# Optimization experiments

Measured on AMD Instinct MI355X. Metric: run time of the kernel, lower is better.

Reference implementation:

```python
import jax, jax.numpy as jnp
import numpy as np

B, D_MODEL, L = 4, 512, 1024
N_HEADS = 8

def setup_inputs() -> dict:
    key = jax.random.key(0)
    ks = jax.random.split(key, 7)
    s = 1.0 / np.sqrt(D_MODEL)
    return {
        "queries": jax.random.normal(ks[0], (B, D_MODEL, 3, L), dtype=jnp.float32),
        "keys":    jax.random.normal(ks[1], (B, D_MODEL, 3, L), dtype=jnp.float32),
        "values":  jax.random.normal(ks[2], (B, D_MODEL, 3, L), dtype=jnp.float32),
        "Wq": jax.random.normal(ks[3], (D_MODEL, D_MODEL), dtype=jnp.float32) * s,
        "Wk": jax.random.normal(ks[4], (D_MODEL, D_MODEL), dtype=jnp.float32) * s,
        "Wv": jax.random.normal(ks[5], (D_MODEL, D_MODEL), dtype=jnp.float32) * s,
        "Wo": jax.random.normal(ks[6], (D_MODEL, D_MODEL), dtype=jnp.float32) * s,
        "n_heads": N_HEADS,
    }

def reference(queries, keys, values, Wq, Wk, Wv, Wo, n_heads):
    # inputs: [B, D, 3, L]; VNLinear = bias-free linear over channel dim D
    Bv, D, _, Lv = queries.shape
    H = n_heads
    dh = D // H
    # project and reshape to [B, L, H, dh, 3]
    def proj(x, W):
        y = jnp.einsum('ed,bdvl->blev', W, x)          # [B, L, D, 3]
        return y.reshape(Bv, Lv, H, dh, 3)
    q = proj(queries, Wq)
    k = proj(keys, Wk)
    v = proj(values, Wv)
    # score over extra vector axis v: [B, H, 3, L, S]
    score = jnp.einsum('blhdv,bshdv->bhvls', q, k)
    scale = 1.0 / jnp.sqrt(jnp.asarray(3.0, score.dtype))  # original grabs last dim (=3)
    attn = jax.nn.softmax(scale * score, axis=-1)
    # weighted values: [B, L, 3, H, dh] -> [B, L, 3, D]
    V = jnp.einsum('bhvls,bshdv->blvhd', attn, v).reshape(Bv, Lv, 3, D)
    # output projection on channel dim: result [B, D, 3, L]
    out = jnp.einsum('ed,blvd->bevl', Wo, V)
    return out, attn
```

## Files before the change

kernel.cpp:

```cpp
#include <hip/hip_runtime.h>
#include <hip/hip_bf16.h>

typedef __hip_bfloat16 bf16;
using bf16x8 = __attribute__((ext_vector_type(8))) short;
using f32x4  = __attribute__((ext_vector_type(4))) float;

#define Bn 4
#define Dm 512
#define Hh 8
#define V3 3
#define Lq 1024
#define NM (Bn*Hh*V3)

#define WPITCH 144

__device__ __forceinline__ unsigned short f2bf(float x) {
    bf16 h = __float2bfloat16(x);
    return *reinterpret_cast<unsigned short*>(&h);
}
__device__ __forceinline__ float bfbits2f(unsigned short u) {
    return __uint_as_float((unsigned)u << 16);
}

constexpr float SCALE = 0.57735026919f;

__global__ __launch_bounds__(256, 4) void proj_all_kernel(
    const float* __restrict__ xq, const float* __restrict__ xk,
    const float* __restrict__ xv,
    const float* __restrict__ Wq, const float* __restrict__ Wk,
    const float* __restrict__ Wv,
    unsigned short* __restrict__ Qh, unsigned short* __restrict__ Ql,
    unsigned short* __restrict__ Kh, unsigned short* __restrict__ Kl,
    unsigned short* __restrict__ Vt)
{
    __shared__ unsigned char Wlds[2 * 64 * WPITCH];
    unsigned char* LWh = Wlds;
    unsigned char* LWl = Wlds + 64 * WPITCH;

    const int fid = (blockIdx.z * gridDim.y + blockIdx.y) * gridDim.x + blockIdx.x;
    const int nid = (fid & 7) * 576 + (fid >> 3);
    const int x_  = nid & 15;
    const int y_  = (nid >> 4) & 7;
    const int zz  = nid >> 7;
    const int pid = zz / 12;
    const int pl  = zz % 12;
    const int b   = pl / V3;
    const int v   = pl % V3;

    const float* xsrc = (pid == 0) ? xq : (pid == 1) ? xk : xv;
    const float* W    = (pid == 0) ? Wq : (pid == 1) ? Wk : Wv;

    const int l0 = x_ * 64;
    const int e0 = y_ * 64;
    const int m  = (b * Hh + y_) * V3 + v;

    const int tid  = threadIdx.x;
    const int w    = tid >> 6;
    const int ln   = tid & 63;
    const int ln15 = ln & 15;
    const int lq   = ln >> 4;
    const int wl   = w * 16 + ln15;

    const float* xbase = xsrc + (size_t)b * Dm * V3 * Lq + (size_t)v * Lq + l0 + wl;

    f32x4 acc[4];
    #pragma unroll
    for (int i = 0; i < 4; ++i) acc[i] = (f32x4)0.f;

    for (int ph = 0; ph < 8; ++ph) {
        const int d0 = ph * 64;

        float xraw[16];
        #pragma unroll
        for (int kq = 0; kq < 2; ++kq)
            #pragma unroll
            for (int j = 0; j < 8; ++j)
                xraw[kq * 8 + j] =
                    xbase[(size_t)(d0 + kq * 32 + lq * 8 + j) * (V3 * Lq)];

        __syncthreads();
        #pragma unroll
        for (int q2 = 0; q2 < 4; ++q2) {
            int idx  = tid + q2 * 256;
            int row  = idx >> 4;
            int dloc = (idx & 15) * 4;
            float4 wv4 = *reinterpret_cast<const float4*>(
                W + (size_t)(e0 + row) * Dm + d0 + dloc);
            float wz[4] = {wv4.x, wv4.y, wv4.z, wv4.w};
            union { unsigned short u[4]; uint2 v2; } hp, lp;
            #pragma unroll
            for (int e = 0; e < 4; ++e) {
                hp.u[e] = f2bf(wz[e]);
                lp.u[e] = f2bf(wz[e] - bfbits2f(hp.u[e]));
            }
            *reinterpret_cast<uint2*>(LWh + row * WPITCH + dloc * 2) = hp.v2;
            *reinterpret_cast<uint2*>(LWl + row * WPITCH + dloc * 2) = lp.v2;
        }
        __syncthreads();

        bf16x8 xh[2], xl[2];
        #pragma unroll
        for (int kq = 0; kq < 2; ++kq)
            #pragma unroll
            for (int j = 0; j < 8; ++j) {
                float xv_ = xraw[kq * 8 + j];
                unsigned short hs = f2bf(xv_);
                unsigned short ls = f2bf(xv_ - bfbits2f(hs));
                xh[kq][j] = (short)hs;
                xl[kq][j] = (short)ls;
            }

        #pragma unroll
        for (int lt = 0; lt < 4; ++lt) {
            int erow = lt * 16 + ln15;
            #pragma unroll
            for (int kq = 0; kq < 2; ++kq) {
                bf16x8 wh = *reinterpret_cast<const bf16x8*>(
                    LWh + erow * WPITCH + kq * 64 + lq * 16);
                bf16x8 wl_ = *reinterpret_cast<const bf16x8*>(
                    LWl + erow * WPITCH + kq * 64 + lq * 16);
                acc[lt] = __builtin_amdgcn_mfma_f32_16x16x32_bf16(wh,  xh[kq], acc[lt], 0, 0, 0);
                acc[lt] = __builtin_amdgcn_mfma_f32_16x16x32_bf16(wl_, xh[kq], acc[lt], 0, 0, 0);
                acc[lt] = __builtin_amdgcn_mfma_f32_16x16x32_bf16(wh,  xl[kq], acc[lt], 0, 0, 0);
            }
        }
    }

    if (pid < 2) {
        unsigned short* Oh_ = (pid == 0) ? Qh : Kh;
        unsigned short* Ol_ = (pid == 0) ? Ql : Kl;
        size_t rowbase = ((size_t)m * Lq + l0 + wl) * 64;
        #pragma unroll
        for (int lt = 0; lt < 4; ++lt) {
            union { unsigned short u[4]; uint2 v2; } hp, lp;
            #pragma unroll
            for (int r = 0; r < 4; ++r) {
                float y = acc[lt][r];
                hp.u[r] = f2bf(y);
                lp.u[r] = f2bf(y - bfbits2f(hp.u[r]));
            }
            *reinterpret_cast<uint2*>(Oh_ + rowbase + lt * 16 + lq * 4) = hp.v2;
            *reinterpret_cast<uint2*>(Ol_ + rowbase + lt * 16 + lq * 4) = lp.v2;
        }
    } else {
        #pragma unroll
        for (int lt = 0; lt < 4; ++lt)
            #pragma unroll
            for (int r = 0; r < 4; ++r) {
                int dd = lt * 16 + lq * 4 + r;
                Vt[(((size_t)(m * 64 + dd)) << 10) + l0 + wl] = f2bf(acc[lt][r]);
            }
    }
}

__device__ __forceinline__ void stage_tile64(
    unsigned char* dst, const unsigned short* __restrict__ src,
    size_t row_stride, int tid)
{
    #pragma unroll
    for (int q = 0; q < 2; ++q) {
        int u = tid + q * 256;
        int row = u >> 3, off = u & 7;
        uint4 d = *reinterpret_cast<const uint4*>(src + (size_t)row * row_stride + off * 8);
        *reinterpret_cast<uint4*>(dst + ((row * 128 + off * 16) ^ ((row & 7) << 4))) = d;
    }
}

__global__ __launch_bounds__(256) void fused_attn_kernel(
    const unsigned short* __restrict__ Qh, const unsigned short* __restrict__ Ql,
    const unsigned short* __restrict__ Kh, const unsigned short* __restrict__ Kl,
    const unsigned short* __restrict__ Vt, float* __restrict__ attn_out,
    unsigned short* __restrict__ Ot)
{
    __shared__ float4 ldsf4[2128];
    unsigned char* L   = (unsigned char*)ldsf4;
    unsigned char* Lkh = L;
    unsigned char* Lkl = L + 8192;
    unsigned char* Lvt = L + 16384;
    unsigned char* Lp  = L + 24576;
    float* rowsumW = (float*)(L + 32768);
    float* invrow  = (float*)(L + 33792);

    const int fid = blockIdx.y * gridDim.x + blockIdx.x;
    const int nid = (fid & 7) * 192 + (fid >> 3);
    const int m  = nid >> 4;
    const int l0 = (nid & 15) * 64;

    const int tid = threadIdx.x;
    const int w    = tid >> 6;
    const int ln   = tid & 63;
    const int ln15 = ln & 15;
    const int lq   = ln >> 4;
    const int sc   = w * 16;

    stage_tile64(Lkh, Qh + ((size_t)m * Lq + l0) * 64, 64, tid);
    stage_tile64(Lkl, Ql + ((size_t)m * Lq + l0) * 64, 64, tid);
    __syncthreads();
    bf16x8 qfh[4][2], qfl[4][2];
    #pragma unroll
    for (int lt = 0; lt < 4; ++lt) {
        int row = lt * 16 + ln15;
        #pragma unroll
        for (int kq = 0; kq < 2; ++kq) {
            int byte = (row * 128 + kq * 64 + lq * 16) ^ ((row & 7) << 4);
            qfh[lt][kq] = *reinterpret_cast<const bf16x8*>(Lkh + byte);
            qfl[lt][kq] = *reinterpret_cast<const bf16x8*>(Lkl + byte);
        }
    }
    __syncthreads();

    const size_t mbase = (size_t)m * Lq * Lq;
    const unsigned short* Khm = Kh + (size_t)m * Lq * 64;
    const unsigned short* Klm = Kl + (size_t)m * Lq * 64;
    const unsigned short* Vtm = Vt + (((size_t)m * 64) << 10);

    float lsum[4][4] = {};
    for (int s0 = 0; s0 < Lq; s0 += 64) {
        stage_tile64(Lkh, Khm + (size_t)s0 * 64, 64, tid);
        stage_tile64(Lkl, Klm + (size_t)s0 * 64, 64, tid);
        __syncthreads();
        bf16x8 bh[2], bl[2];
        #pragma unroll
        for (int kq = 0; kq < 2; ++kq) {
            int row = sc + ln15;
            int byte = (row * 128 + kq * 64 + lq * 16) ^ ((row & 7) << 4);
            bh[kq] = *reinterpret_cast<const bf16x8*>(Lkh + byte);
            bl[kq] = *reinterpret_cast<const bf16x8*>(Lkl + byte);
        }
        #pragma unroll
        for (int lt = 0; lt < 4; ++lt) {
            f32x4 c = (f32x4)0.f;
            #pragma unroll
            for (int kq = 0; kq < 2; ++kq) {
                c = __builtin_amdgcn_mfma_f32_16x16x32_bf16(qfh[lt][kq], bh[kq], c, 0, 0, 0);
                c = __builtin_amdgcn_mfma_f32_16x16x32_bf16(qfl[lt][kq], bh[kq], c, 0, 0, 0);
                c = __builtin_amdgcn_mfma_f32_16x16x32_bf16(qfh[lt][kq], bl[kq], c, 0, 0, 0);
            }
            #pragma unroll
            for (int r = 0; r < 4; ++r)
                lsum[lt][r] += __expf(c[r] * SCALE);
        }
        __syncthreads();
    }
    #pragma unroll
    for (int lt = 0; lt < 4; ++lt)
        #pragma unroll
        for (int r = 0; r < 4; ++r) {
            float vv = lsum[lt][r];
            vv += __shfl_xor(vv, 1);
            vv += __shfl_xor(vv, 2);
            vv += __shfl_xor(vv, 4);
            vv += __shfl_xor(vv, 8);
            if (ln15 == 0) rowsumW[w * 64 + lt * 16 + lq * 4 + r] = vv;
        }
    __syncthreads();
    if (tid < 64)
        invrow[tid] = 1.0f / (rowsumW[tid] + rowsumW[64 + tid] +
                              rowsumW[128 + tid] + rowsumW[192 + tid]);
    __syncthreads();

    f32x4 o[4];
    o[0] = (f32x4)0.f; o[1] = (f32x4)0.f; o[2] = (f32x4)0.f; o[3] = (f32x4)0.f;

    const int arow = tid >> 2;
    const int acb  = (tid & 3) * 32;
    const int aswz = (arow & 7) << 4;

    for (int s0 = 0; s0 < Lq; s0 += 64) {
        stage_tile64(Lkh, Khm + (size_t)s0 * 64, 64, tid);
        stage_tile64(Lkl, Klm + (size_t)s0 * 64, 64, tid);
        stage_tile64(Lvt, Vtm + s0, 1024, tid);
        __syncthreads();
        bf16x8 bh[2], bl[2];
        #pragma unroll
        for (int kq = 0; kq < 2; ++kq) {
            int row = sc + ln15;
            int byte = (row * 128 + kq * 64 + lq * 16) ^ ((row & 7) << 4);
            bh[kq] = *reinterpret_cast<const bf16x8*>(Lkh + byte);
            bl[kq] = *reinterpret_cast<const bf16x8*>(Lkl + byte);
        }
        #pragma unroll
        for (int lt = 0; lt < 4; ++lt) {
            f32x4 c = (f32x4)0.f;
            #pragma unroll
            for (int kq = 0; kq < 2; ++kq) {
                c = __builtin_amdgcn_mfma_f32_16x16x32_bf16(qfh[lt][kq], bh[kq], c, 0, 0, 0);
                c = __builtin_amdgcn_mfma_f32_16x16x32_bf16(qfl[lt][kq], bh[kq], c, 0, 0, 0);
                c = __builtin_amdgcn_mfma_f32_16x16x32_bf16(qfh[lt][kq], bl[kq], c, 0, 0, 0);
            }
            #pragma unroll
            for (int r = 0; r < 4; ++r) {
                int l = lt * 16 + lq * 4 + r;
                float p = __expf(c[r] * SCALE) * invrow[l];
                int byte = (l * 128 + (sc + ln15) * 2) ^ ((l & 7) << 4);
                *reinterpret_cast<unsigned short*>(Lp + byte) = f2bf(p);
            }
        }
        __syncthreads();
        {
            int prow = w * 16 + ln15;
            #pragma unroll
            for (int kq = 0; kq < 2; ++kq) {
                bf16x8 pa = *reinterpret_cast<const bf16x8*>(
                    Lp + ((prow * 128 + kq * 64 + lq * 16) ^ ((prow & 7) << 4)));
                #pragma unroll
                for (int nt = 0; nt < 4; ++nt) {
                    int vrow = nt * 16 + ln15;
                    bf16x8 vb = *reinterpret_cast<const bf16x8*>(
                        Lvt + ((vrow * 128 + kq * 64 + lq * 16) ^ ((vrow & 7) << 4)));
                    o[nt] = __builtin_amdgcn_mfma_f32_16x16x32_bf16(pa, vb, o[nt], 0, 0, 0);
                }
            }
        }
        {
            bf16x8 p0 = *reinterpret_cast<const bf16x8*>(
                Lp + ((arow * 128 + acb) ^ aswz));
            bf16x8 p1 = *reinterpret_cast<const bf16x8*>(
                Lp + ((arow * 128 + acb + 16) ^ aswz));
            float* dst = attn_out + mbase + (size_t)(l0 + arow) * Lq + s0 + (tid & 3) * 16;
            float4 f;
            f.x = bfbits2f((unsigned short)p0[0]);
            f.y = bfbits2f((unsigned short)p0[1]);
            f.z = bfbits2f((unsigned short)p0[2]);
            f.w = bfbits2f((unsigned short)p0[3]);
            *reinterpret_cast<float4*>(dst) = f;
            f.x = bfbits2f((unsigned short)p0[4]);
            f.y = bfbits2f((unsigned short)p0[5]);
            f.z = bfbits2f((unsigned short)p0[6]);
            f.w = bfbits2f((unsigned short)p0[7]);
            *reinterpret_cast<float4*>(dst + 4) = f;
            f.x = bfbits2f((unsigned short)p1[0]);
            f.y = bfbits2f((unsigned short)p1[1]);
            f.z = bfbits2f((unsigned short)p1[2]);
            f.w = bfbits2f((unsigned short)p1[3]);
            *reinterpret_cast<float4*>(dst + 8) = f;
            f.x = bfbits2f((unsigned short)p1[4]);
            f.y = bfbits2f((unsigned short)p1[5]);
            f.z = bfbits2f((unsigned short)p1[6]);
            f.w = bfbits2f((unsigned short)p1[7]);
            *reinterpret_cast<float4*>(dst + 12) = f;
        }
        __syncthreads();
    }

    #pragma unroll
    for (int nt = 0; nt < 4; ++nt) {
        int dd = nt * 16 + ln15;
        #pragma unroll
        for (int r = 0; r < 4; ++r) {
            int l = w * 16 + lq * 4 + r;
            Ot[((size_t)m * Lq + l0 + l) * 64 + dd] = f2bf(o[nt][r]);
        }
    }
}

__global__ __launch_bounds__(256, 4) void oproj_kernel(
    const float* __restrict__ Wo, const unsigned short* __restrict__ Ot,
    float* __restrict__ out)
{
    __shared__ unsigned char Wlds[2 * 64 * WPITCH];
    unsigned char* LWh = Wlds;
    unsigned char* LWl = Wlds + 64 * WPITCH;

    const int fid = (blockIdx.z * gridDim.y + blockIdx.y) * gridDim.x + blockIdx.x;
    const int nid = (fid & 7) * 192 + (fid >> 3);
    const int x_  = nid & 15;
    const int y_  = (nid >> 4) & 7;
    const int pl  = nid >> 7;
    const int b   = pl / V3;
    const int v   = pl % V3;

    const int l0 = x_ * 64;
    const int e0 = y_ * 64;

    const int tid  = threadIdx.x;
    const int w    = tid >> 6;
    const int ln   = tid & 63;
    const int ln15 = ln & 15;
    const int lq   = ln >> 4;
    const int wl   = w * 16 + ln15;

    f32x4 acc[4];
    #pragma unroll
    for (int i = 0; i < 4; ++i) acc[i] = (f32x4)0.f;

    for (int h = 0; h < Hh; ++h) {
        const int m = (b * Hh + h) * V3 + v;

        size_t obase = ((size_t)m * Lq + l0 + wl) * 64;
        bf16x8 ob0 = *reinterpret_cast<const bf16x8*>(Ot + obase + lq * 8);
        bf16x8 ob1 = *reinterpret_cast<const bf16x8*>(Ot + obase + 32 + lq * 8);

        __syncthreads();
        #pragma unroll
        for (int q2 = 0; q2 < 4; ++q2) {
            int idx  = tid + q2 * 256;
            int row  = idx >> 4;
            int dloc = (idx & 15) * 4;
            float4 wv4 = *reinterpret_cast<const float4*>(
                Wo + (size_t)(e0 + row) * Dm + h * 64 + dloc);
            float wz[4] = {wv4.x, wv4.y, wv4.z, wv4.w};
            union { unsigned short u[4]; uint2 v2; } hp, lp;
            #pragma unroll
            for (int e = 0; e < 4; ++e) {
                hp.u[e] = f2bf(wz[e]);
                lp.u[e] = f2bf(wz[e] - bfbits2f(hp.u[e]));
            }
            *reinterpret_cast<uint2*>(LWh + row * WPITCH + dloc * 2) = hp.v2;
            *reinterpret_cast<uint2*>(LWl + row * WPITCH + dloc * 2) = lp.v2;
        }
        __syncthreads();

        #pragma unroll
        for (int lt = 0; lt < 4; ++lt) {
            int erow = lt * 16 + ln15;
            #pragma unroll
            for (int kq = 0; kq < 2; ++kq) {
                bf16x8 wh = *reinterpret_cast<const bf16x8*>(
                    LWh + erow * WPITCH + kq * 64 + lq * 16);
                bf16x8 wl_ = *reinterpret_cast<const bf16x8*>(
                    LWl + erow * WPITCH + kq * 64 + lq * 16);
                bf16x8 ob = kq ? ob1 : ob0;
                acc[lt] = __builtin_amdgcn_mfma_f32_16x16x32_bf16(wh,  ob, acc[lt], 0, 0, 0);
                acc[lt] = __builtin_amdgcn_mfma_f32_16x16x32_bf16(wl_, ob, acc[lt], 0, 0, 0);
            }
        }
    }

    #pragma unroll
    for (int lt = 0; lt < 4; ++lt)
        #pragma unroll
        for (int r = 0; r < 4; ++r) {
            int e = e0 + lt * 16 + lq * 4 + r;
            out[((size_t)(b * Dm + e) * V3 + v) * Lq + l0 + wl] = acc[lt][r];
        }
}

extern "C" void kernel_launch(void* const* d_in, const int* in_sizes, int n_in,
                              void* d_out, int out_size, void* d_ws, size_t ws_size,
                              hipStream_t stream)
{
    const float* q  = (const float*)d_in[0];
    const float* k  = (const float*)d_in[1];
    const float* vv = (const float*)d_in[2];
    const float* Wq = (const float*)d_in[3];
    const float* Wk = (const float*)d_in[4];
    const float* Wv = (const float*)d_in[5];
    const float* Wo = (const float*)d_in[6];

    float* out      = (float*)d_out;
    float* attn_out = out + (size_t)Bn * Dm * V3 * Lq;

    char* w = (char*)d_ws;
    unsigned short* Qh = (unsigned short*)(w);
    unsigned short* Ql = (unsigned short*)(w + 12582912);
    unsigned short* Kh = (unsigned short*)(w + 25165824);
    unsigned short* Kl = (unsigned short*)(w + 37748736);
    unsigned short* Vt = (unsigned short*)(w + 50331648);
    unsigned short* Ot = (unsigned short*)(w + 62914560);

    dim3 b256(256);

    proj_all_kernel<<<dim3(16, 8, 36), b256, 0, stream>>>(
        q, k, vv, Wq, Wk, Wv, Qh, Ql, Kh, Kl, Vt);

    fused_attn_kernel<<<dim3(16, NM), b256, 0, stream>>>(
        Qh, Ql, Kh, Kl, Vt, attn_out, Ot);

    oproj_kernel<<<dim3(16, 8, 12), b256, 0, stream>>>(Wo, Ot, out);
}
```

Measured before the change: 721.7 us.

## Pre-split weights once and share K/V tiles across two query blocks

A new kernel splits all four weight matrices into bf16 hi/lo planes once per call. The projection kernels then copy pre-split bf16 tiles into LDS instead of converting fp32 weights in every block. The attention kernel now uses 512-thread blocks that cover 128 query rows as two 64-row halves, so each staged K/V tile serves twice as many queries and global K/V traffic is halved. This adds a kernel launch and uses more LDS per block, which may lower occupancy.

```diff
diff --git a/kernel.cpp b/kernel.cpp
--- a/kernel.cpp
+++ b/kernel.cpp
@@ -24,11 +24,31 @@
 
 constexpr float SCALE = 0.57735026919f;
 
+__global__ __launch_bounds__(256) void split_w_kernel(
+    const float* __restrict__ Wq, const float* __restrict__ Wk,
+    const float* __restrict__ Wv, const float* __restrict__ Wo,
+    unsigned short* __restrict__ Wsp)
+{
+    const int mi = blockIdx.x >> 8;
+    const float* src = (mi == 0) ? Wq : (mi == 1) ? Wk : (mi == 2) ? Wv : Wo;
+    const int idx = ((blockIdx.x & 255) << 8) + threadIdx.x;
+    float4 v4 = reinterpret_cast<const float4*>(src)[idx];
+    float z[4] = {v4.x, v4.y, v4.z, v4.w};
+    union { unsigned short u[4]; uint2 q; } hp, lp;
+    #pragma unroll
+    for (int e = 0; e < 4; ++e) {
+        hp.u[e] = f2bf(z[e]);
+        lp.u[e] = f2bf(z[e] - bfbits2f(hp.u[e]));
+    }
+    unsigned short* hi = Wsp + (size_t)mi * 524288;
+    *reinterpret_cast<uint2*>(hi + (size_t)idx * 4)          = hp.q;
+    *reinterpret_cast<uint2*>(hi + 262144 + (size_t)idx * 4) = lp.q;
+}
+
 __global__ __launch_bounds__(256, 4) void proj_all_kernel(
     const float* __restrict__ xq, const float* __restrict__ xk,
     const float* __restrict__ xv,
-    const float* __restrict__ Wq, const float* __restrict__ Wk,
-    const float* __restrict__ Wv,
+    const unsigned short* __restrict__ Wsp,
     unsigned short* __restrict__ Qh, unsigned short* __restrict__ Ql,
     unsigned short* __restrict__ Kh, unsigned short* __restrict__ Kl,
     unsigned short* __restrict__ Vt)
@@ -48,7 +68,8 @@
     const int v   = pl % V3;
 
     const float* xsrc = (pid == 0) ? xq : (pid == 1) ? xk : xv;
-    const float* W    = (pid == 0) ? Wq : (pid == 1) ? Wk : Wv;
+    const unsigned short* WhX = Wsp + (size_t)pid * 524288;
+    const unsigned short* WlX = WhX + 262144;
 
     const int l0 = x_ * 64;
     const int e0 = y_ * 64;
@@ -81,20 +102,14 @@
         __syncthreads();
         #pragma unroll
         for (int q2 = 0; q2 < 4; ++q2) {
-            int idx  = tid + q2 * 256;
-            int row  = idx >> 4;
-            int dloc = (idx & 15) * 4;
-            float4 wv4 = *reinterpret_cast<const float4*>(
-                W + (size_t)(e0 + row) * Dm + d0 + dloc);
-            float wz[4] = {wv4.x, wv4.y, wv4.z, wv4.w};
-            union { unsigned short u[4]; uint2 v2; } hp, lp;
-            #pragma unroll
-            for (int e = 0; e < 4; ++e) {
-                hp.u[e] = f2bf(wz[e]);
-                lp.u[e] = f2bf(wz[e] - bfbits2f(hp.u[e]));
-            }
-            *reinterpret_cast<uint2*>(LWh + row * WPITCH + dloc * 2) = hp.v2;
-            *reinterpret_cast<uint2*>(LWl + row * WPITCH + dloc * 2) = lp.v2;
+            int idx = tid + q2 * 256;
+            const unsigned short* srcw = (idx < 512) ? WhX : WlX;
+            unsigned char* dstw = (idx < 512) ? LWh : LWl;
+            int i = idx & 511;
+            int row = i >> 3, off = i & 7;
+            uint4 d = *reinterpret_cast<const uint4*>(
+                srcw + (size_t)(e0 + row) * Dm + d0 + off * 8);
+            *reinterpret_cast<uint4*>(dstw + row * WPITCH + off * 16) = d;
         }
         __syncthreads();
 
@@ -153,49 +168,54 @@
     }
 }
 
-__device__ __forceinline__ void stage_tile64(
+__device__ __forceinline__ void stage512(
     unsigned char* dst, const unsigned short* __restrict__ src,
     size_t row_stride, int tid)
 {
-    #pragma unroll
-    for (int q = 0; q < 2; ++q) {
-        int u = tid + q * 256;
-        int row = u >> 3, off = u & 7;
-        uint4 d = *reinterpret_cast<const uint4*>(src + (size_t)row * row_stride + off * 8);
-        *reinterpret_cast<uint4*>(dst + ((row * 128 + off * 16) ^ ((row & 7) << 4))) = d;
-    }
-}
-
-__global__ __launch_bounds__(256) void fused_attn_kernel(
+    int row = tid >> 3, off = tid & 7;
+    uint4 d = *reinterpret_cast<const uint4*>(src + (size_t)row * row_stride + off * 8);
+    *reinterpret_cast<uint4*>(dst + ((row * 128 + off * 16) ^ ((row & 7) << 4))) = d;
+}
+
+__global__ __launch_bounds__(512, 4) void fused_attn_kernel(
     const unsigned short* __restrict__ Qh, const unsigned short* __restrict__ Ql,
     const unsigned short* __restrict__ Kh, const unsigned short* __restrict__ Kl,
     const unsigned short* __restrict__ Vt, float* __restrict__ attn_out,
     unsigned short* __restrict__ Ot)
 {
-    __shared__ float4 ldsf4[2128];
+    __shared__ float4 ldsf4[2720];
     unsigned char* L   = (unsigned char*)ldsf4;
     unsigned char* Lkh = L;
     unsigned char* Lkl = L + 8192;
     unsigned char* Lvt = L + 16384;
     unsigned char* Lp  = L + 24576;
-    float* rowsumW = (float*)(L + 32768);
-    float* invrow  = (float*)(L + 33792);
+    float* rowsumW = (float*)(L + 40960);
+    float* invrow  = (float*)(L + 43008);
 
     const int fid = blockIdx.y * gridDim.x + blockIdx.x;
-    const int nid = (fid & 7) * 192 + (fid >> 3);
-    const int m  = nid >> 4;
-    const int l0 = (nid & 15) * 64;
-
-    const int tid = threadIdx.x;
-    const int w    = tid >> 6;
+    const int nid = (fid & 7) * 96 + (fid >> 3);
+    const int m   = nid >> 3;
+    const int l0b = (nid & 7) * 128;
+
+    const int tid  = threadIdx.x;
+    const int hw   = tid >> 8;
+    const int t8   = tid & 255;
+    const int w    = t8 >> 6;
     const int ln   = tid & 63;
     const int ln15 = ln & 15;
     const int lq   = ln >> 4;
     const int sc   = w * 16;
-
-    stage_tile64(Lkh, Qh + ((size_t)m * Lq + l0) * 64, 64, tid);
-    stage_tile64(Lkl, Ql + ((size_t)m * Lq + l0) * 64, 64, tid);
+    const int lh0  = l0b + hw * 64;
+
+    unsigned char* Lph = Lp + hw * 8192;
+
+    stage512(Lkh, Qh + ((size_t)m * Lq + l0b) * 64, 64, tid);
+    stage512(Lkl, Ql + ((size_t)m * Lq + l0b) * 64, 64, tid);
+    stage512(Lvt, Qh + ((size_t)m * Lq + l0b + 64) * 64, 64, tid);
+    stage512(Lp,  Ql + ((size_t)m * Lq + l0b + 64) * 64, 64, tid);
     __syncthreads();
+    const unsigned char* Lqh_ = hw ? Lvt : Lkh;
+    const unsigned char* Lql_ = hw ? Lp  : Lkl;
     bf16x8 qfh[4][2], qfl[4][2];
     #pragma unroll
     for (int lt = 0; lt < 4; ++lt) {
@@ -203,8 +223,8 @@
         #pragma unroll
         for (int kq = 0; kq < 2; ++kq) {
             int byte = (row * 128 + kq * 64 + lq * 16) ^ ((row & 7) << 4);
-            qfh[lt][kq] = *reinterpret_cast<const bf16x8*>(Lkh + byte);
-            qfl[lt][kq] = *reinterpret_cast<const bf16x8*>(Lkl + byte);
+            qfh[lt][kq] = *reinterpret_cast<const bf16x8*>(Lqh_ + byte);
+            qfl[lt][kq] = *reinterpret_cast<const bf16x8*>(Lql_ + byte);
         }
     }
     __syncthreads();
@@ -216,8 +236,8 @@
 
     float lsum[4][4] = {};
     for (int s0 = 0; s0 < Lq; s0 += 64) {
-        stage_tile64(Lkh, Khm + (size_t)s0 * 64, 64, tid);
-        stage_tile64(Lkl, Klm + (size_t)s0 * 64, 64, tid);
+        stage512(Lkh, Khm + (size_t)s0 * 64, 64, tid);
+        stage512(Lkl, Klm + (size_t)s0 * 64, 64, tid);
         __syncthreads();
         bf16x8 bh[2], bl[2];
         #pragma unroll
@@ -251,25 +271,28 @@
             vv += __shfl_xor(vv, 2);
             vv += __shfl_xor(vv, 4);
             vv += __shfl_xor(vv, 8);
-            if (ln15 == 0) rowsumW[w * 64 + lt * 16 + lq * 4 + r] = vv;
+            if (ln15 == 0)
+                rowsumW[(hw * 4 + w) * 64 + lt * 16 + lq * 4 + r] = vv;
         }
     __syncthreads();
-    if (tid < 64)
-        invrow[tid] = 1.0f / (rowsumW[tid] + rowsumW[64 + tid] +
-                              rowsumW[128 + tid] + rowsumW[192 + tid]);
+    if (t8 < 64) {
+        float* rs = rowsumW + hw * 256;
+        invrow[hw * 64 + t8] = 1.0f /
+            (rs[t8] + rs[64 + t8] + rs[128 + t8] + rs[192 + t8]);
+    }
     __syncthreads();
 
     f32x4 o[4];
     o[0] = (f32x4)0.f; o[1] = (f32x4)0.f; o[2] = (f32x4)0.f; o[3] = (f32x4)0.f;
 
-    const int arow = tid >> 2;
-    const int acb  = (tid & 3) * 32;
+    const int arow = t8 >> 2;
+    const int acb  = (t8 & 3) * 32;
     const int aswz = (arow & 7) << 4;
 
     for (int s0 = 0; s0 < Lq; s0 += 64) {
-        stage_tile64(Lkh, Khm + (size_t)s0 * 64, 64, tid);
-        stage_tile64(Lkl, Klm + (size_t)s0 * 64, 64, tid);
-        stage_tile64(Lvt, Vtm + s0, 1024, tid);
+        stage512(Lkh, Khm + (size_t)s0 * 64, 64, tid);
+        stage512(Lkl, Klm + (size_t)s0 * 64, 64, tid);
+        stage512(Lvt, Vtm + s0, 1024, tid);
         __syncthreads();
         bf16x8 bh[2], bl[2];
         #pragma unroll
@@ -291,9 +314,9 @@
             #pragma unroll
             for (int r = 0; r < 4; ++r) {
                 int l = lt * 16 + lq * 4 + r;
-                float p = __expf(c[r] * SCALE) * invrow[l];
+                float p = __expf(c[r] * SCALE) * invrow[hw * 64 + l];
                 int byte = (l * 128 + (sc + ln15) * 2) ^ ((l & 7) << 4);
-                *reinterpret_cast<unsigned short*>(Lp + byte) = f2bf(p);
+                *reinterpret_cast<unsigned short*>(Lph + byte) = f2bf(p);
             }
         }
         __syncthreads();
@@ -302,7 +325,7 @@
             #pragma unroll
             for (int kq = 0; kq < 2; ++kq) {
                 bf16x8 pa = *reinterpret_cast<const bf16x8*>(
-                    Lp + ((prow * 128 + kq * 64 + lq * 16) ^ ((prow & 7) << 4)));
+                    Lph + ((prow * 128 + kq * 64 + lq * 16) ^ ((prow & 7) << 4)));
                 #pragma unroll
                 for (int nt = 0; nt < 4; ++nt) {
                     int vrow = nt * 16 + ln15;
@@ -314,10 +337,10 @@
         }
         {
             bf16x8 p0 = *reinterpret_cast<const bf16x8*>(
-                Lp + ((arow * 128 + acb) ^ aswz));
+                Lph + ((arow * 128 + acb) ^ aswz));
             bf16x8 p1 = *reinterpret_cast<const bf16x8*>(
-                Lp + ((arow * 128 + acb + 16) ^ aswz));
-            float* dst = attn_out + mbase + (size_t)(l0 + arow) * Lq + s0 + (tid & 3) * 16;
+                Lph + ((arow * 128 + acb + 16) ^ aswz));
+            float* dst = attn_out + mbase + (size_t)(lh0 + arow) * Lq + s0 + (t8 & 3) * 16;
             float4 f;
             f.x = bfbits2f((unsigned short)p0[0]);
             f.y = bfbits2f((unsigned short)p0[1]);
@@ -349,18 +372,21 @@
         #pragma unroll
         for (int r = 0; r < 4; ++r) {
             int l = w * 16 + lq * 4 + r;
-            Ot[((size_t)m * Lq + l0 + l) * 64 + dd] = f2bf(o[nt][r]);
+            Ot[((size_t)m * Lq + lh0 + l) * 64 + dd] = f2bf(o[nt][r]);
         }
     }
 }
 
 __global__ __launch_bounds__(256, 4) void oproj_kernel(
-    const float* __restrict__ Wo, const unsigned short* __restrict__ Ot,
+    const unsigned short* __restrict__ Wsp, const unsigned short* __restrict__ Ot,
     float* __restrict__ out)
 {
     __shared__ unsigned char Wlds[2 * 64 * WPITCH];
     unsigned char* LWh = Wlds;
     unsigned char* LWl = Wlds + 64 * WPITCH;
+
+    const unsigned short* WhO = Wsp + (size_t)3 * 524288;
+    const unsigned short* WlO = WhO + 262144;
 
     const int fid = (blockIdx.z * gridDim.y + blockIdx.y) * gridDim.x + blockIdx.x;
     const int nid = (fid & 7) * 192 + (fid >> 3);
@@ -394,20 +420,14 @@
         __syncthreads();
         #pragma unroll
         for (int q2 = 0; q2 < 4; ++q2) {
-            int idx  = tid + q2 * 256;
-            int row  = idx >> 4;
-            int dloc = (idx & 15) * 4;
-            float4 wv4 = *reinterpret_cast<const float4*>(
-                Wo + (size_t)(e0 + row) * Dm + h * 64 + dloc);
-            float wz[4] = {wv4.x, wv4.y, wv4.z, wv4.w};
-            union { unsigned short u[4]; uint2 v2; } hp, lp;
-            #pragma unroll
-            for (int e = 0; e < 4; ++e) {
-                hp.u[e] = f2bf(wz[e]);
-                lp.u[e] = f2bf(wz[e] - bfbits2f(hp.u[e]));
-            }
-            *reinterpret_cast<uint2*>(LWh + row * WPITCH + dloc * 2) = hp.v2;
-            *reinterpret_cast<uint2*>(LWl + row * WPITCH + dloc * 2) = lp.v2;
+            int idx = tid + q2 * 256;
+            const unsigned short* srcw = (idx < 512) ? WhO : WlO;
+            unsigned char* dstw = (idx < 512) ? LWh : LWl;
+            int i = idx & 511;
+            int row = i >> 3, off = i & 7;
+            uint4 d = *reinterpret_cast<const uint4*>(
+                srcw + (size_t)(e0 + row) * Dm + h * 64 + off * 8);
+            *reinterpret_cast<uint4*>(dstw + row * WPITCH + off * 16) = d;
         }
         __syncthreads();
 
@@ -452,20 +472,23 @@
     float* attn_out = out + (size_t)Bn * Dm * V3 * Lq;
 
     char* w = (char*)d_ws;
-    unsigned short* Qh = (unsigned short*)(w);
-    unsigned short* Ql = (unsigned short*)(w + 12582912);
-    unsigned short* Kh = (unsigned short*)(w + 25165824);
-    unsigned short* Kl = (unsigned short*)(w + 37748736);
-    unsigned short* Vt = (unsigned short*)(w + 50331648);
-    unsigned short* Ot = (unsigned short*)(w + 62914560);
+    unsigned short* Qh  = (unsigned short*)(w);
+    unsigned short* Ql  = (unsigned short*)(w + 12582912);
+    unsigned short* Kh  = (unsigned short*)(w + 25165824);
+    unsigned short* Kl  = (unsigned short*)(w + 37748736);
+    unsigned short* Vt  = (unsigned short*)(w + 50331648);
+    unsigned short* Ot  = (unsigned short*)(w + 62914560);
+    unsigned short* Wsp = (unsigned short*)(w + 75497472);
 
     dim3 b256(256);
 
+    split_w_kernel<<<dim3(1024), b256, 0, stream>>>(Wq, Wk, Wv, Wo, Wsp);
+
     proj_all_kernel<<<dim3(16, 8, 36), b256, 0, stream>>>(
-        q, k, vv, Wq, Wk, Wv, Qh, Ql, Kh, Kl, Vt);
-
-    fused_attn_kernel<<<dim3(16, NM), b256, 0, stream>>>(
+        q, k, vv, Wsp, Qh, Ql, Kh, Kl, Vt);
+
+    fused_attn_kernel<<<dim3(8, NM), dim3(512), 0, stream>>>(
         Qh, Ql, Kh, Kl, Vt, attn_out, Ot);
 
-    oproj_kernel<<<dim3(16, 8, 12), b256, 0, stream>>>(Wo, Ot, out);
-}
+    oproj_kernel<<<dim3(16, 8, 12), b256, 0, stream>>>(Wsp, Ot, out);
+}
```

Result: slower. 790.6 us (+9.5%).
